# Kernel tuning notes

Hardware: AMD Instinct MI355X
Metric: run time of the kernel (lower is better)

The kernel has to match this reference:

```python
import jax, jax.numpy as jnp
import numpy as np

N = 50000
GAMMA = 0.1

def spmm(row, col, val, x):
    # sparse [N,N] @ dense [N,D] via gather + segment-sum over destination rows
    return jax.ops.segment_sum(val[:, None] * x[col], row, num_segments=N)

def setup_inputs() -> dict:
    key = jax.random.key(0)
    ks = jax.random.split(key, 16)
    E, EK, F, H, C = 800000, 1000000, 512, 128, 40
    return {
        "fea": jax.random.normal(ks[0], (N, F), jnp.float32),
        "adj_row": jax.random.randint(ks[1], (E,), 0, N),
        "adj_col": jax.random.randint(ks[2], (E,), 0, N),
        "adj_val": jax.random.uniform(ks[3], (E,), jnp.float32),
        "knn_row": jax.random.randint(ks[4], (EK,), 0, N),
        "knn_col": jax.random.randint(ks[5], (EK,), 0, N),
        "knn_val": jax.random.uniform(ks[6], (EK,), jnp.float32),
        "W1": jax.random.normal(ks[7], (F, H), jnp.float32) * (1.0 / np.sqrt(F)),
        "b1": jnp.zeros((H,), jnp.float32),
        "W2": jax.random.normal(ks[8], (H, C), jnp.float32) * (1.0 / np.sqrt(H)),
        "b2": jnp.zeros((C,), jnp.float32),
        "score1": jax.random.normal(ks[9], (F, 1), jnp.float32),
        "score2": jax.random.normal(ks[10], (H, 1), jnp.float32),
        "sbias1": jnp.zeros((1,), jnp.float32),
        "sbias2": jnp.zeros((1,), jnp.float32),
        "Dk1": jax.random.normal(ks[11], (F, 1), jnp.float32),
        "Dk2": jax.random.normal(ks[12], (H, 1), jnp.float32),
        "Dbias1": jnp.zeros((1,), jnp.float32),
        "Dbias2": jnp.zeros((1,), jnp.float32),
    }

def simpgcn_layer(x, W, b, s_w, s_b, d_w, d_b, adj_row, adj_col, adj_val, knn_row, knn_col, knn_val):
    support = x @ W                     # [N, Dout] shared across the 3 adjacencies
    h_adj = spmm(adj_row, adj_col, adj_val, support) + b
    h_knn = spmm(knn_row, knn_col, knn_val, support) + b
    h_id = support + b                  # identity adjacency: spmm(I, support)
    s = jax.nn.sigmoid(x @ s_w + s_b)   # [N,1] learned self-loop gate
    Dk = x @ d_w + d_b                  # [N,1]
    return s * h_adj + (1.0 - s) * h_knn + GAMMA * Dk * h_id

def reference(fea, adj_row, adj_col, adj_val, knn_row, knn_col, knn_val,
              W1, b1, W2, b2, score1, score2, sbias1, sbias2,
              Dk1, Dk2, Dbias1, Dbias2):
    x = simpgcn_layer(fea, W1, b1, score1, sbias1, Dk1, Dbias1,
                      adj_row, adj_col, adj_val, knn_row, knn_col, knn_val)
    embedding = x  # dropout is identity in eval mode
    x = simpgcn_layer(x, W2, b2, score2, sbias2, Dk2, Dbias2,
                      adj_row, adj_col, adj_val, knn_row, knn_col, knn_val)
    return jax.nn.log_softmax(x, axis=1), embedding
```

## Files before the change

kernel.cpp:

```cpp
#include <hip/hip_runtime.h>
#include <hip/hip_bf16.h>
#include <cstdint>

#define GAMMA 0.1f
#define CAP 64
#define OVF_CAP 16384

typedef unsigned int  uint32;
typedef unsigned short ushort16;
typedef float f32x4 __attribute__((ext_vector_type(4)));
typedef __bf16 bf16x8 __attribute__((ext_vector_type(8)));

union U16x8 { uint4 u4; bf16x8 bv; };

static __device__ __forceinline__ ushort16 f2bf(float f) {
    union { float f; uint32 u; } x; x.f = f;
    uint32 r = (x.u + 0x7FFFu + ((x.u >> 16) & 1u)) >> 16;
    return (ushort16)r;
}
static __device__ __forceinline__ uint32 pack2bf(float lo, float hi) {
    return (uint32)f2bf(lo) | ((uint32)f2bf(hi) << 16);
}
static __device__ __forceinline__ float bflo(uint32 u) { return __uint_as_float(u << 16); }
static __device__ __forceinline__ float bfhi(uint32 u) { return __uint_as_float(u & 0xFFFF0000u); }

__global__ __launch_bounds__(256) void prep_wt(const float* __restrict__ W1,
                                               const float* __restrict__ W2,
                                               ushort16* __restrict__ W1bt,
                                               ushort16* __restrict__ W2bt,
                                               int* __restrict__ cnt, int NC) {
    int t = blockIdx.x * 256 + threadIdx.x;
    if (t < 128 * 512) { int c = t >> 9, k = t & 511; W1bt[t] = f2bf(W1[k * 128 + c]); }
    if (t < 48 * 128)  { int c = t >> 7, k = t & 127; W2bt[t] = f2bf(c < 40 ? W2[k * 40 + c] : 0.f); }
    for (int j = t; j < NC; j += 256 * 256) cnt[j] = 0;
}

__global__ __launch_bounds__(256) void gemm1_scatter(
    const float* __restrict__ A, const ushort16* __restrict__ Bt,
    const float* __restrict__ s1w, const float* __restrict__ d1w,
    const float* __restrict__ s1b, const float* __restrict__ d1b,
    ushort16* __restrict__ Cb, float* __restrict__ s_out, float* __restrict__ dk_out,
    int M, int mgrid,
    const int* __restrict__ arow_, const int* __restrict__ acol_, const float* __restrict__ aval_, int E,
    const int* __restrict__ krow_, const int* __restrict__ kcol_, const float* __restrict__ kval_, int EK,
    int* __restrict__ cnt, int N,
    uint32* __restrict__ packed_a, uint32* __restrict__ packed_k,
    uint2* __restrict__ ovf_a, uint2* __restrict__ ovf_k) {
    int bid = blockIdx.x;
    if (bid >= mgrid) {
        int i = (bid - mgrid) * 256 + threadIdx.x;
        if (i < E) {
            int r = arow_[i];
            uint32 vb = (uint32)f2bf(aval_[i]);
            uint32 rec = ((uint32)acol_[i] << 16) | vb;
            int p = atomicAdd(&cnt[r], 1);
            if (p < CAP) __builtin_nontemporal_store(rec, &packed_a[(size_t)r * CAP + p]);
            else { int q = atomicAdd(&cnt[2 * N], 1); if (q < OVF_CAP) ovf_a[q] = make_uint2((uint32)r, (uint32)acol_[i] | (vb << 16)); }
        }
        if (i < EK) {
            int r = krow_[i];
            uint32 vb = (uint32)f2bf(kval_[i]);
            uint32 rec = ((uint32)kcol_[i] << 16) | vb;
            int p = atomicAdd(&cnt[N + r], 1);
            if (p < CAP) __builtin_nontemporal_store(rec, &packed_k[(size_t)r * CAP + p]);
            else { int q = atomicAdd(&cnt[2 * N + 1], 1); if (q < OVF_CAP) ovf_k[q] = make_uint2((uint32)r, (uint32)kcol_[i] | (vb << 16)); }
        }
        return;
    }
    int w = threadIdx.x >> 6, lane = threadIdx.x & 63;
    int row16 = lane & 15, kc = lane >> 4;
    int wrow0 = bid * 64 + w * 16;
    int r = wrow0 + row16;
    int rc = min(r, M - 1);
    const float* arow = A + (size_t)rc * 512;

    f32x4 acc[8];
    #pragma unroll
    for (int c = 0; c < 8; ++c) acc[c] = (f32x4){0.f, 0.f, 0.f, 0.f};
    float sdot = 0.f, ddot = 0.f;

    for (int ks = 0; ks < 16; ++ks) {
        int kb = ks * 32 + kc * 8;
        float4 a0 = *reinterpret_cast<const float4*>(arow + kb);
        float4 a1 = *reinterpret_cast<const float4*>(arow + kb + 4);
        float4 sw0 = *reinterpret_cast<const float4*>(s1w + kb);
        float4 sw1 = *reinterpret_cast<const float4*>(s1w + kb + 4);
        float4 dw0 = *reinterpret_cast<const float4*>(d1w + kb);
        float4 dw1 = *reinterpret_cast<const float4*>(d1w + kb + 4);
        sdot += a0.x * sw0.x + a0.y * sw0.y + a0.z * sw0.z + a0.w * sw0.w +
                a1.x * sw1.x + a1.y * sw1.y + a1.z * sw1.z + a1.w * sw1.w;
        ddot += a0.x * dw0.x + a0.y * dw0.y + a0.z * dw0.z + a0.w * dw0.w +
                a1.x * dw1.x + a1.y * dw1.y + a1.z * dw1.z + a1.w * dw1.w;
        U16x8 ua;
        ua.u4 = make_uint4(pack2bf(a0.x, a0.y), pack2bf(a0.z, a0.w),
                           pack2bf(a1.x, a1.y), pack2bf(a1.z, a1.w));
        #pragma unroll
        for (int c = 0; c < 8; ++c) {
            U16x8 ub;
            ub.u4 = *reinterpret_cast<const uint4*>(Bt + (size_t)(c * 16 + row16) * 512 + kb);
            acc[c] = __builtin_amdgcn_mfma_f32_16x16x32_bf16(ua.bv, ub.bv, acc[c], 0, 0, 0);
        }
    }

    sdot += __shfl_xor(sdot, 16); sdot += __shfl_xor(sdot, 32);
    ddot += __shfl_xor(ddot, 16); ddot += __shfl_xor(ddot, 32);
    if (kc == 0 && r < M) {
        s_out[r] = 1.f / (1.f + __expf(-(sdot + s1b[0])));
        dk_out[r] = ddot + d1b[0];
    }

    #pragma unroll
    for (int c = 0; c < 8; ++c) {
        #pragma unroll
        for (int i = 0; i < 4; ++i) {
            int orow = wrow0 + (lane >> 4) * 4 + i;
            if (orow < M) Cb[(size_t)orow * 128 + c * 16 + row16] = f2bf(acc[c][i]);
        }
    }
}

__global__ __launch_bounds__(256) void gemm2_mfma(const ushort16* __restrict__ Ab,
                                                  const ushort16* __restrict__ Bt,
                                                  float* __restrict__ C,
                                                  ushort16* __restrict__ Cb,
                                                  int M) {
    int w = threadIdx.x >> 6, lane = threadIdx.x & 63;
    int row16 = lane & 15, kc = lane >> 4;
    int wrow0 = blockIdx.x * 64 + w * 16;
    int r = wrow0 + row16;
    int rc = min(r, M - 1);

    f32x4 acc[3];
    #pragma unroll
    for (int c = 0; c < 3; ++c) acc[c] = (f32x4){0.f, 0.f, 0.f, 0.f};

    #pragma unroll
    for (int ks = 0; ks < 4; ++ks) {
        int kb = ks * 32 + kc * 8;
        U16x8 ua;
        ua.u4 = *reinterpret_cast<const uint4*>(Ab + (size_t)rc * 128 + kb);
        #pragma unroll
        for (int c = 0; c < 3; ++c) {
            U16x8 ub;
            ub.u4 = *reinterpret_cast<const uint4*>(Bt + (size_t)(c * 16 + row16) * 128 + kb);
            acc[c] = __builtin_amdgcn_mfma_f32_16x16x32_bf16(ua.bv, ub.bv, acc[c], 0, 0, 0);
        }
    }

    #pragma unroll
    for (int c = 0; c < 3; ++c) {
        int col = c * 16 + row16;
        #pragma unroll
        for (int i = 0; i < 4; ++i) {
            int orow = wrow0 + (lane >> 4) * 4 + i;
            if (orow < M && col < 40) {
                C[(size_t)orow * 40 + col] = acc[c][i];
                Cb[(size_t)orow * 40 + col] = f2bf(acc[c][i]);
            }
        }
    }
}

__global__ __launch_bounds__(256) void spmm_combine1(
    const int* __restrict__ cnt,
    const uint32* __restrict__ packed_a, const uint32* __restrict__ packed_k,
    const uint2* __restrict__ ovf_a, const uint2* __restrict__ ovf_k,
    const ushort16* __restrict__ supb, const float* __restrict__ s, const float* __restrict__ dk,
    const float* __restrict__ b1,
    const float* __restrict__ s2w, const float* __restrict__ d2w,
    const float* __restrict__ s2b, const float* __restrict__ d2b,
    float* __restrict__ emb, ushort16* __restrict__ embb,
    float* __restrict__ s_out, float* __restrict__ dk_out, int N) {
    int w = threadIdx.x >> 6, l = threadIdx.x & 63;
    int r = blockIdx.x * 4 + w;
    if (r >= N) return;
    const uint32* su = (const uint32*)supb;

    float a0 = 0.f, a1 = 0.f, k0 = 0.f, k1 = 0.f;
    {
        const uint32* pa = packed_a + (size_t)r * CAP;
        int d = min(cnt[r], CAP);
        for (int e = 0; e < d; e += 8) {
            uint32 rec[8], uu[8];
            #pragma unroll
            for (int j = 0; j < 8; ++j) rec[j] = pa[min(e + j, d - 1)];
            #pragma unroll
            for (int j = 0; j < 8; ++j) uu[j] = su[((size_t)(rec[j] >> 16) << 6) + l];
            #pragma unroll
            for (int j = 0; j < 8; ++j) {
                float v = (e + j < d) ? bflo(rec[j]) : 0.f;
                a0 += v * bflo(uu[j]); a1 += v * bfhi(uu[j]);
            }
        }
    }
    {
        const uint32* pk = packed_k + (size_t)r * CAP;
        int d = min(cnt[N + r], CAP);
        for (int e = 0; e < d; e += 8) {
            uint32 rec[8], uu[8];
            #pragma unroll
            for (int j = 0; j < 8; ++j) rec[j] = pk[min(e + j, d - 1)];
            #pragma unroll
            for (int j = 0; j < 8; ++j) uu[j] = su[((size_t)(rec[j] >> 16) << 6) + l];
            #pragma unroll
            for (int j = 0; j < 8; ++j) {
                float v = (e + j < d) ? bflo(rec[j]) : 0.f;
                k0 += v * bflo(uu[j]); k1 += v * bfhi(uu[j]);
            }
        }
    }
    int nova = min(cnt[2 * N], OVF_CAP);
    for (int i = 0; i < nova; ++i) {
        uint2 t = ovf_a[i];
        if ((int)t.x != r) continue;
        float v = bfhi(t.y);
        uint32 u = su[((size_t)(t.y & 0xFFFFu) << 6) + l];
        a0 += v * bflo(u); a1 += v * bfhi(u);
    }
    int novk = min(cnt[2 * N + 1], OVF_CAP);
    for (int i = 0; i < novk; ++i) {
        uint2 t = ovf_k[i];
        if ((int)t.x != r) continue;
        float v = bfhi(t.y);
        uint32 u = su[((size_t)(t.y & 0xFFFFu) << 6) + l];
        k0 += v * bflo(u); k1 += v * bfhi(u);
    }

    float si = s[r];
    float g = GAMMA * dk[r];
    uint32 ui = su[((size_t)r << 6) + l];
    int c0i = l * 2, c1i = l * 2 + 1;
    float o0 = si * a0 + (1.f - si) * k0 + g * bflo(ui) + b1[c0i] * (1.f + g);
    float o1 = si * a1 + (1.f - si) * k1 + g * bfhi(ui) + b1[c1i] * (1.f + g);

    *reinterpret_cast<float2*>(emb + (size_t)r * 128 + c0i) = make_float2(o0, o1);
    ((uint32*)embb)[((size_t)r << 6) + l] = pack2bf(o0, o1);

    float as = o0 * s2w[c0i] + o1 * s2w[c1i];
    float ad = o0 * d2w[c0i] + o1 * d2w[c1i];
    #pragma unroll
    for (int off = 32; off; off >>= 1) {
        as += __shfl_xor(as, off);
        ad += __shfl_xor(ad, off);
    }
    if (l == 0) {
        s_out[r] = 1.f / (1.f + __expf(-(as + s2b[0])));
        dk_out[r] = ad + d2b[0];
    }
}

__global__ __launch_bounds__(256) void spmm_combine2_lsm(
    const int* __restrict__ cnt,
    const uint32* __restrict__ packed_a, const uint32* __restrict__ packed_k,
    const uint2* __restrict__ ovf_a, const uint2* __restrict__ ovf_k,
    const ushort16* __restrict__ supb, const float* __restrict__ supf,
    const float* __restrict__ s, const float* __restrict__ dk,
    const float* __restrict__ b2, float* __restrict__ out, int N) {
    int w = threadIdx.x >> 6, l = threadIdx.x & 63;
    int r = blockIdx.x * 4 + w;
    if (r >= N) return;
    int g = (l >= 40) ? 2 : ((l >= 20) ? 1 : 0);
    int li = l - g * 20;
    bool act = l < 60;
    const uint32* su = (const uint32*)supb;

    float a0 = 0.f, a1 = 0.f, k0 = 0.f, k1 = 0.f;
    {
        const uint32* pa = packed_a + (size_t)r * CAP;
        int d = min(cnt[r], CAP);
        for (int e = 0; e < d; e += 6) {
            uint32 rr[6];
            #pragma unroll
            for (int j = 0; j < 6; ++j) rr[j] = pa[min(e + j, d - 1)];
            uint32 rca = (g == 0) ? rr[0] : ((g == 1) ? rr[1] : rr[2]);
            uint32 rcb = (g == 0) ? rr[3] : ((g == 1) ? rr[4] : rr[5]);
            uint32 ua = su[(size_t)(rca >> 16) * 20 + li];
            uint32 ub = su[(size_t)(rcb >> 16) * 20 + li];
            float va = (act && (e + g) < d) ? bflo(rca) : 0.f;
            float vb = (act && (e + 3 + g) < d) ? bflo(rcb) : 0.f;
            a0 += va * bflo(ua) + vb * bflo(ub);
            a1 += va * bfhi(ua) + vb * bfhi(ub);
        }
    }
    {
        const uint32* pk = packed_k + (size_t)r * CAP;
        int d = min(cnt[N + r], CAP);
        for (int e = 0; e < d; e += 6) {
            uint32 rr[6];
            #pragma unroll
            for (int j = 0; j < 6; ++j) rr[j] = pk[min(e + j, d - 1)];
            uint32 rca = (g == 0) ? rr[0] : ((g == 1) ? rr[1] : rr[2]);
            uint32 rcb = (g == 0) ? rr[3] : ((g == 1) ? rr[4] : rr[5]);
            uint32 ua = su[(size_t)(rca >> 16) * 20 + li];
            uint32 ub = su[(size_t)(rcb >> 16) * 20 + li];
            float va = (act && (e + g) < d) ? bflo(rca) : 0.f;
            float vb = (act && (e + 3 + g) < d) ? bflo(rcb) : 0.f;
            k0 += va * bflo(ua) + vb * bflo(ub);
            k1 += va * bfhi(ua) + vb * bfhi(ub);
        }
    }
    {
        float t1, t2;
        t1 = __shfl(a0, (l + 20) & 63); t2 = __shfl(a0, (l + 40) & 63); a0 += t1 + t2;
        t1 = __shfl(a1, (l + 20) & 63); t2 = __shfl(a1, (l + 40) & 63); a1 += t1 + t2;
        t1 = __shfl(k0, (l + 20) & 63); t2 = __shfl(k0, (l + 40) & 63); k0 += t1 + t2;
        t1 = __shfl(k1, (l + 20) & 63); t2 = __shfl(k1, (l + 40) & 63); k1 += t1 + t2;
    }
    int nova = min(cnt[2 * N], OVF_CAP);
    for (int i = 0; i < nova; ++i) {
        uint2 t = ovf_a[i];
        if ((int)t.x != r) continue;
        if (l < 20) {
            float v = bfhi(t.y);
            uint32 u = su[(size_t)(t.y & 0xFFFFu) * 20 + l];
            a0 += v * bflo(u); a1 += v * bfhi(u);
        }
    }
    int novk = min(cnt[2 * N + 1], OVF_CAP);
    for (int i = 0; i < novk; ++i) {
        uint2 t = ovf_k[i];
        if ((int)t.x != r) continue;
        if (l < 20) {
            float v = bfhi(t.y);
            uint32 u = su[(size_t)(t.y & 0xFFFFu) * 20 + l];
            k0 += v * bflo(u); k1 += v * bfhi(u);
        }
    }

    float si = s[r];
    float gg = GAMMA * dk[r];
    float z0 = -INFINITY, z1 = -INFINITY;
    if (l < 20) {
        float2 iv = *reinterpret_cast<const float2*>(supf + (size_t)r * 40 + l * 2);
        z0 = si * a0 + (1.f - si) * k0 + gg * iv.x + b2[l * 2] * (1.f + gg);
        z1 = si * a1 + (1.f - si) * k1 + gg * iv.y + b2[l * 2 + 1] * (1.f + gg);
    }
    float m = fmaxf(z0, z1);
    #pragma unroll
    for (int off = 16; off; off >>= 1) m = fmaxf(m, __shfl_xor(m, off));
    float ex = (l < 20) ? (__expf(z0 - m) + __expf(z1 - m)) : 0.f;
    #pragma unroll
    for (int off = 16; off; off >>= 1) ex += __shfl_xor(ex, off);
    float lse = m + __logf(ex);
    if (l < 20)
        *reinterpret_cast<float2*>(out + (size_t)r * 40 + l * 2) = make_float2(z0 - lse, z1 - lse);
}

static inline size_t align256(size_t x) { return (x + 255) & ~(size_t)255; }

extern "C" void kernel_launch(void* const* d_in, const int* in_sizes, int n_in,
                              void* d_out, int out_size, void* d_ws, size_t ws_size,
                              hipStream_t stream) {
    const int N = 50000, C = 40;

    const float* fea     = (const float*)d_in[0];
    const int*   adj_row = (const int*)d_in[1];
    const int*   adj_col = (const int*)d_in[2];
    const float* adj_val = (const float*)d_in[3];
    const int*   knn_row = (const int*)d_in[4];
    const int*   knn_col = (const int*)d_in[5];
    const float* knn_val = (const float*)d_in[6];
    const float* W1      = (const float*)d_in[7];
    const float* b1      = (const float*)d_in[8];
    const float* W2      = (const float*)d_in[9];
    const float* b2      = (const float*)d_in[10];
    const float* score1  = (const float*)d_in[11];
    const float* score2  = (const float*)d_in[12];
    const float* sbias1  = (const float*)d_in[13];
    const float* sbias2  = (const float*)d_in[14];
    const float* Dk1     = (const float*)d_in[15];
    const float* Dk2     = (const float*)d_in[16];
    const float* Dbias1  = (const float*)d_in[17];
    const float* Dbias2  = (const float*)d_in[18];

    const int E  = in_sizes[1];
    const int EK = in_sizes[4];

    float* out_lsm = (float*)d_out;
    float* emb     = out_lsm + (size_t)N * C;

    char* wp = (char*)d_ws;
    ushort16* W1bt = (ushort16*)wp; wp += align256((size_t)128 * 512 * 2);
    ushort16* W2bt = (ushort16*)wp; wp += align256((size_t)48 * 128 * 2);
    char* sup1_region = wp;          wp += align256((size_t)N * 128 * 2);
    ushort16* sup1b = (ushort16*)sup1_region;
    float* sup2     = (float*)sup1_region;
    ushort16* sup2b = (ushort16*)(sup1_region + (size_t)N * 40 * 4);
    ushort16* embb  = (ushort16*)wp; wp += align256((size_t)N * 128 * 2);
    float* s_buf  = (float*)wp; wp += align256((size_t)N * 4);
    float* dk_buf = (float*)wp; wp += align256((size_t)N * 4);
    int* cnt  = (int*)wp; wp += align256((size_t)(2 * N + 2) * 4);
    uint32* packed_a = (uint32*)wp; wp += align256((size_t)N * CAP * 4);
    uint32* packed_k = (uint32*)wp; wp += align256((size_t)N * CAP * 4);
    uint2* ovf_a = (uint2*)wp; wp += align256((size_t)OVF_CAP * 8);
    uint2* ovf_k = (uint2*)wp; wp += align256((size_t)OVF_CAP * 8);

    int egrid = (max(E, EK) + 255) / 256;
    int mgrid = (N + 63) / 64;

    prep_wt<<<256, 256, 0, stream>>>(W1, W2, W1bt, W2bt, cnt, 2 * N + 2);

    gemm1_scatter<<<mgrid + egrid, 256, 0, stream>>>(
        fea, W1bt, score1, Dk1, sbias1, Dbias1, sup1b, s_buf, dk_buf, N, mgrid,
        adj_row, adj_col, adj_val, E, knn_row, knn_col, knn_val, EK,
        cnt, N, packed_a, packed_k, ovf_a, ovf_k);

    spmm_combine1<<<(N + 3) / 4, 256, 0, stream>>>(cnt, packed_a, packed_k, ovf_a, ovf_k,
                                                   sup1b, s_buf, dk_buf, b1,
                                                   score2, Dk2, sbias2, Dbias2,
                                                   emb, embb, s_buf, dk_buf, N);

    gemm2_mfma<<<mgrid, 256, 0, stream>>>(embb, W2bt, sup2, sup2b, N);

    spmm_combine2_lsm<<<(N + 3) / 4, 256, 0, stream>>>(cnt, packed_a, packed_k, ovf_a, ovf_k,
                                                       sup2b, sup2, s_buf, dk_buf,
                                                       b2, out_lsm, N);

    (void)n_in; (void)out_size; (void)ws_size;
}
```

Measured before the change: 488.0 us.

## Two-pass bucketed edge scatter: coarse row-block arena then per-block LDS binning

```diff
diff --git a/kernel.cpp b/kernel.cpp
--- a/kernel.cpp
+++ b/kernel.cpp
@@ -5,6 +5,10 @@
 #define GAMMA 0.1f
 #define CAP 64
 #define OVF_CAP 16384
+#define NROWB 256
+#define NBK 196
+#define NSUBX 8
+#define CAPSEG 1536
 
 typedef unsigned int  uint32;
 typedef unsigned short ushort16;
@@ -28,11 +32,13 @@
                                                const float* __restrict__ W2,
                                                ushort16* __restrict__ W1bt,
                                                ushort16* __restrict__ W2bt,
-                                               int* __restrict__ cnt, int NC) {
+                                               int* __restrict__ gcur,
+                                               int* __restrict__ ovfc) {
     int t = blockIdx.x * 256 + threadIdx.x;
     if (t < 128 * 512) { int c = t >> 9, k = t & 511; W1bt[t] = f2bf(W1[k * 128 + c]); }
     if (t < 48 * 128)  { int c = t >> 7, k = t & 127; W2bt[t] = f2bf(c < 40 ? W2[k * 40 + c] : 0.f); }
-    for (int j = t; j < NC; j += 256 * 256) cnt[j] = 0;
+    if (t < NBK * NSUBX) gcur[t] = 0;
+    if (t < 2) ovfc[t] = 0;
 }
 
 __global__ __launch_bounds__(256) void gemm1_scatter(
@@ -43,27 +49,31 @@
     int M, int mgrid,
     const int* __restrict__ arow_, const int* __restrict__ acol_, const float* __restrict__ aval_, int E,
     const int* __restrict__ krow_, const int* __restrict__ kcol_, const float* __restrict__ kval_, int EK,
-    int* __restrict__ cnt, int N,
-    uint32* __restrict__ packed_a, uint32* __restrict__ packed_k,
+    int* __restrict__ gcur, uint2* __restrict__ arena, int* __restrict__ ovfc,
     uint2* __restrict__ ovf_a, uint2* __restrict__ ovf_k) {
     int bid = blockIdx.x;
     if (bid >= mgrid) {
         int i = (bid - mgrid) * 256 + threadIdx.x;
+        int sub = bid & (NSUBX - 1);
         if (i < E) {
             int r = arow_[i];
+            int col = acol_[i];
             uint32 vb = (uint32)f2bf(aval_[i]);
-            uint32 rec = ((uint32)acol_[i] << 16) | vb;
-            int p = atomicAdd(&cnt[r], 1);
-            if (p < CAP) __builtin_nontemporal_store(rec, &packed_a[(size_t)r * CAP + p]);
-            else { int q = atomicAdd(&cnt[2 * N], 1); if (q < OVF_CAP) ovf_a[q] = make_uint2((uint32)r, (uint32)acol_[i] | (vb << 16)); }
+            int slot = (r >> 8) * NSUBX + sub;
+            int p = atomicAdd(&gcur[slot], 1);
+            if (p < CAPSEG)
+                arena[(size_t)slot * CAPSEG + p] = make_uint2((uint32)r, ((uint32)col << 16) | vb);
+            else { int q = atomicAdd(&ovfc[0], 1); if (q < OVF_CAP) ovf_a[q] = make_uint2((uint32)r, (uint32)col | (vb << 16)); }
         }
         if (i < EK) {
             int r = krow_[i];
+            int col = kcol_[i];
             uint32 vb = (uint32)f2bf(kval_[i]);
-            uint32 rec = ((uint32)kcol_[i] << 16) | vb;
-            int p = atomicAdd(&cnt[N + r], 1);
-            if (p < CAP) __builtin_nontemporal_store(rec, &packed_k[(size_t)r * CAP + p]);
-            else { int q = atomicAdd(&cnt[2 * N + 1], 1); if (q < OVF_CAP) ovf_k[q] = make_uint2((uint32)r, (uint32)kcol_[i] | (vb << 16)); }
+            int slot = (r >> 8) * NSUBX + sub;
+            int p = atomicAdd(&gcur[slot], 1);
+            if (p < CAPSEG)
+                arena[(size_t)slot * CAPSEG + p] = make_uint2((uint32)r | 0x10000u, ((uint32)col << 16) | vb);
+            else { int q = atomicAdd(&ovfc[1], 1); if (q < OVF_CAP) ovf_k[q] = make_uint2((uint32)r, (uint32)col | (vb << 16)); }
         }
         return;
     }
@@ -119,6 +129,45 @@
     }
 }
 
+__global__ __launch_bounds__(256) void scatter_p2(
+    const int* __restrict__ gcur, const uint2* __restrict__ arena,
+    uint32* __restrict__ packed_a, uint32* __restrict__ packed_k,
+    int* __restrict__ cnt, int* __restrict__ ovfc,
+    uint2* __restrict__ ovf_a, uint2* __restrict__ ovf_k, int N) {
+    int b = blockIdx.x;
+    __shared__ int lc[2 * NROWB];
+    for (int j = threadIdx.x; j < 2 * NROWB; j += 256) lc[j] = 0;
+    __syncthreads();
+
+    int row0 = b * NROWB;
+    for (int sub = 0; sub < NSUBX; ++sub) {
+        int slot = b * NSUBX + sub;
+        const uint2* seg = arena + (size_t)slot * CAPSEG;
+        int c = min(gcur[slot], CAPSEG);
+        for (int i = threadIdx.x; i < c; i += 256) {
+            uint2 rec = seg[i];
+            int r = (int)(rec.x & 0xFFFFu);
+            int type = (int)(rec.x >> 16);
+            int p = atomicAdd(&lc[type * NROWB + (r - row0)], 1);
+            if (p < CAP) {
+                (type ? packed_k : packed_a)[(size_t)r * CAP + p] = rec.y;
+            } else {
+                uint32 col = rec.y >> 16, vb = rec.y & 0xFFFFu;
+                int q = atomicAdd(&ovfc[type], 1);
+                if (q < OVF_CAP) (type ? ovf_k : ovf_a)[q] = make_uint2((uint32)r, col | (vb << 16));
+            }
+        }
+    }
+    __syncthreads();
+    for (int j = threadIdx.x; j < NROWB; j += 256) {
+        int r = row0 + j;
+        if (r < N) {
+            cnt[r]     = lc[j];
+            cnt[N + r] = lc[NROWB + j];
+        }
+    }
+}
+
 __global__ __launch_bounds__(256) void gemm2_mfma(const ushort16* __restrict__ Ab,
                                                   const ushort16* __restrict__ Bt,
                                                   float* __restrict__ C,
@@ -394,16 +443,22 @@
     uint32* packed_k = (uint32*)wp; wp += align256((size_t)N * CAP * 4);
     uint2* ovf_a = (uint2*)wp; wp += align256((size_t)OVF_CAP * 8);
     uint2* ovf_k = (uint2*)wp; wp += align256((size_t)OVF_CAP * 8);
+    int* gcur = (int*)wp; wp += align256((size_t)NBK * NSUBX * 4);
+    uint2* arena = (uint2*)wp; wp += align256((size_t)NBK * NSUBX * CAPSEG * 8);
+    int* ovfc = cnt + 2 * N;
 
     int egrid = (max(E, EK) + 255) / 256;
     int mgrid = (N + 63) / 64;
 
-    prep_wt<<<256, 256, 0, stream>>>(W1, W2, W1bt, W2bt, cnt, 2 * N + 2);
+    prep_wt<<<256, 256, 0, stream>>>(W1, W2, W1bt, W2bt, gcur, ovfc);
 
     gemm1_scatter<<<mgrid + egrid, 256, 0, stream>>>(
         fea, W1bt, score1, Dk1, sbias1, Dbias1, sup1b, s_buf, dk_buf, N, mgrid,
         adj_row, adj_col, adj_val, E, knn_row, knn_col, knn_val, EK,
-        cnt, N, packed_a, packed_k, ovf_a, ovf_k);
+        gcur, arena, ovfc, ovf_a, ovf_k);
+
+    scatter_p2<<<NBK, 256, 0, stream>>>(gcur, arena, packed_a, packed_k,
+                                        cnt, ovfc, ovf_a, ovf_k, N);
 
     spmm_combine1<<<(N + 3) / 4, 256, 0, stream>>>(cnt, packed_a, packed_k, ovf_a, ovf_k,
                                                    sup1b, s_buf, dk_buf, b1,
```

Result: slower. 695.7 us (+42.6%).
